# Kernel tuning notes

Measured on AMD Instinct MI355X. Metric: run time of the kernel, lower is better.

The kernel has to match this reference:

```python
import math
import jax, jax.numpy as jnp
import numpy as np

B, S, D = 64, 729, 64  # S = (32*14//16 - 1)**2

def setup_inputs() -> dict:
    key = jax.random.key(0)
    kq, kk, kv, km = jax.random.split(key, 4)
    return {
        "query": jax.random.normal(kq, (B, S, D), dtype=jnp.float32),
        "key": jax.random.normal(kk, (B, S, D), dtype=jnp.float32),
        "value": jax.random.normal(kv, (B, S, D), dtype=jnp.float32),
        "mask": jax.random.randint(km, (B, S, S), 0, 2, dtype=jnp.int32),
    }

def reference(query, key, value, mask):
    dk = query.shape[-1]
    # [B,S,S] scores
    scores = jnp.einsum('bqd,bkd->bqk', query, key) / math.sqrt(dk)
    scores = jnp.where(mask == 0, jnp.float32(-1e9), scores)
    attention = jnp.tanh(scores)  # args.activation == 'tanh'
    # ignore_diag == 1: zero the diagonal of each [S,S] attention map
    eye = jnp.eye(attention.shape[-1], dtype=attention.dtype)
    attention = attention * (1.0 - eye)
    out = jnp.einsum('bqk,bkd->bqd', attention, value)
    return (out, attention)
```

## Files before the change

### kernel.cpp

```cpp
#include <hip/hip_runtime.h>

#define BATCH 64
#define SEQ 729
#define DIM 64
#define NT 12
#define STRB 72
#define STRW 68

typedef __attribute__((ext_vector_type(8))) short bf16x8;
typedef __attribute__((ext_vector_type(4))) float f32x4;
typedef int   i32x4a __attribute__((ext_vector_type(4), aligned(4)));
typedef float f32x4a __attribute__((ext_vector_type(4), aligned(4)));

__device__ __forceinline__ unsigned short f2bf(float f) {
    unsigned int u = __float_as_uint(f);
    u += 0x7fffu + ((u >> 16) & 1u);
    return (unsigned short)(u >> 16);
}

__device__ __forceinline__ unsigned long long pack4bf(float a, float b, float c, float d) {
    return (unsigned long long)f2bf(a)
         | ((unsigned long long)f2bf(b) << 16)
         | ((unsigned long long)f2bf(c) << 32)
         | ((unsigned long long)f2bf(d) << 48);
}

__device__ __forceinline__ float fast_tanh(float x) {
    float e = __builtin_amdgcn_exp2f(x * 2.88539008177792681f);
    return 1.0f - 2.0f * __builtin_amdgcn_rcpf(e + 1.0f);
}

__global__ __launch_bounds__(256, 3) void attn_kernel(
    const float* __restrict__ Qg, const float* __restrict__ Kg,
    const float* __restrict__ Vg, const int* __restrict__ Mg,
    float* __restrict__ Og, float* __restrict__ Ag)
{
    __shared__ unsigned short Ks[64 * STRB];
    __shared__ unsigned short Vs[64 * STRB];
    __shared__ unsigned short Qs[64 * STRB];
    __shared__ float Pf[64 * STRW];
    int* Mint = (int*)Pf;

    const int tid = threadIdx.x;
    const int q0  = blockIdx.x * 64;
    const int b   = blockIdx.y;

    const float* Qb = Qg + (size_t)b * SEQ * DIM;
    const float* Kb = Kg + (size_t)b * SEQ * DIM;
    const float* Vb = Vg + (size_t)b * SEQ * DIM;
    const int*   Mb = Mg + (size_t)b * SEQ * SEQ;
    float* Ob = Og + (size_t)b * SEQ * DIM;
    float* Ab = Ag + (size_t)b * SEQ * SEQ;

    const int lane = tid & 63;
    const int quad = lane >> 4;
    const int l15  = lane & 15;
    const int qrow = (tid >> 6) * 16;

    const int rr = tid >> 4;
    const int cc = (tid & 15) * 4;
    const int vd0 = (tid & 15) * 4;
    const int vk0 = (tid >> 4) * 4;
    const int prow = qrow + (lane >> 4);
    const int pcol = (lane & 15) * 4;

    float4 kr[4], vr[4];
    i32x4a mr[4];

    auto load_k = [&](int k0n) {
        #pragma unroll
        for (int i = 0; i < 4; ++i) {
            int gk = k0n + rr + 16 * i;
            kr[i] = (gk < SEQ) ? *(const float4*)(Kb + gk * DIM + cc)
                               : float4{0, 0, 0, 0};
        }
    };
    auto load_v = [&](int k0n) {
        #pragma unroll
        for (int i = 0; i < 4; ++i) {
            int gk = k0n + vk0 + i;
            vr[i] = (gk < SEQ) ? *(const float4*)(Vb + gk * DIM + vd0)
                               : float4{0, 0, 0, 0};
        }
    };
    auto load_mask = [&](int k0n) {
        #pragma unroll
        for (int i = 0; i < 4; ++i) {
            int gq = q0 + prow + 4 * i;
            int gk = k0n + pcol;
            if (gq < SEQ && gk + 3 < SEQ) {
                mr[i] = *(const i32x4a*)(Mb + (size_t)gq * SEQ + gk);
            } else if (gq < SEQ) {
                i32x4a t;
                #pragma unroll
                for (int e = 0; e < 4; ++e)
                    t[e] = (gk + e < SEQ) ? Mb[(size_t)gq * SEQ + gk + e] : 0;
                mr[i] = t;
            } else {
                mr[i] = i32x4a{0, 0, 0, 0};
            }
        }
    };
    auto drain_mask = [&]() {
        #pragma unroll
        for (int i = 0; i < 4; ++i)
            *(i32x4a*)&Mint[(prow + 4 * i) * STRW + pcol] = mr[i];
    };
    auto drain_kv = [&]() {
        #pragma unroll
        for (int i = 0; i < 4; ++i)
            *(unsigned long long*)&Ks[(rr + 16 * i) * STRB + cc] =
                pack4bf(kr[i].x, kr[i].y, kr[i].z, kr[i].w);
        #pragma unroll
        for (int j = 0; j < 4; ++j) {
            float v0 = j==0?vr[0].x:j==1?vr[0].y:j==2?vr[0].z:vr[0].w;
            float v1 = j==0?vr[1].x:j==1?vr[1].y:j==2?vr[1].z:vr[1].w;
            float v2 = j==0?vr[2].x:j==1?vr[2].y:j==2?vr[2].z:vr[2].w;
            float v3 = j==0?vr[3].x:j==1?vr[3].y:j==2?vr[3].z:vr[3].w;
            *(unsigned long long*)&Vs[(vd0 + j) * STRB + vk0] = pack4bf(v0, v1, v2, v3);
        }
    };

    #pragma unroll
    for (int i = 0; i < 4; ++i) {
        int gq = q0 + rr + 16 * i;
        float4 x = (gq < SEQ) ? *(const float4*)(Qb + gq * DIM + cc)
                              : float4{0, 0, 0, 0};
        *(unsigned long long*)&Qs[(rr + 16 * i) * STRB + cc] = pack4bf(x.x, x.y, x.z, x.w);
    }
    __syncthreads();

    const bf16x8 aq0 = *(const bf16x8*)&Qs[(qrow + l15) * STRB + quad * 8];
    const bf16x8 aq1 = *(const bf16x8*)&Qs[(qrow + l15) * STRB + 32 + quad * 8];

    load_k(0); load_v(0); load_mask(0);

    f32x4 oacc[4];
    #pragma unroll
    for (int dt = 0; dt < 4; ++dt) {
        oacc[dt][0]=0.f; oacc[dt][1]=0.f; oacc[dt][2]=0.f; oacc[dt][3]=0.f;
    }

    for (int kt = 0; kt < NT; ++kt) {
        const int k0 = kt * 64;

        __syncthreads();
        drain_mask();
        drain_kv();
        __syncthreads();

        if (kt + 1 < NT) {
            load_k(k0 + 64); load_v(k0 + 64); load_mask(k0 + 64);
        }

        f32x4 sacc[4];
        #pragma unroll
        for (int nt2 = 0; nt2 < 4; ++nt2) {
            bf16x8 bk0 = *(const bf16x8*)&Ks[(nt2 * 16 + l15) * STRB + quad * 8];
            bf16x8 bk1 = *(const bf16x8*)&Ks[(nt2 * 16 + l15) * STRB + 32 + quad * 8];
            f32x4 c; c[0]=0.f; c[1]=0.f; c[2]=0.f; c[3]=0.f;
            c = __builtin_amdgcn_mfma_f32_16x16x32_bf16(aq0, bk0, c, 0, 0, 0);
            c = __builtin_amdgcn_mfma_f32_16x16x32_bf16(aq1, bk1, c, 0, 0, 0);
            sacc[nt2] = c;
        }

        #pragma unroll
        for (int nt2 = 0; nt2 < 4; ++nt2) {
            int col = nt2 * 16 + l15;
            int gk  = k0 + col;
            #pragma unroll
            for (int r = 0; r < 4; ++r) {
                int qloc = qrow + quad * 4 + r;
                int gq = q0 + qloc;
                int m = Mint[qloc * STRW + col];
                float sv = sacc[nt2][r] * 0.125f;
                bool msk = (m == 0);
                float p = fast_tanh(msk ? -1e9f : sv);
                if (msk) p = -1.0f;
                if (gq == gk) p = 0.0f;
                if (gq >= SEQ || gk >= SEQ) p = 0.0f;
                Pf[qloc * STRW + col] = p;
                Qs[qloc * STRB + col] = f2bf(p);
            }
        }

        #pragma unroll
        for (int i = 0; i < 4; ++i) {
            int row = prow + 4 * i;
            int gq  = q0 + row;
            int gk  = k0 + pcol;
            f32x4 pv = *(const f32x4*)&Pf[row * STRW + pcol];
            if (gq < SEQ) {
                if (gk + 3 < SEQ) {
                    *(f32x4a*)(Ab + (size_t)gq * SEQ + gk) = pv;
                } else {
                    #pragma unroll
                    for (int e = 0; e < 4; ++e)
                        if (gk + e < SEQ) Ab[(size_t)gq * SEQ + gk + e] = pv[e];
                }
            }
        }

        const bf16x8 ap0 = *(const bf16x8*)&Qs[(qrow + l15) * STRB + quad * 8];
        const bf16x8 ap1 = *(const bf16x8*)&Qs[(qrow + l15) * STRB + 32 + quad * 8];
        #pragma unroll
        for (int dt = 0; dt < 4; ++dt) {
            bf16x8 bv0 = *(const bf16x8*)&Vs[(dt * 16 + l15) * STRB + quad * 8];
            bf16x8 bv1 = *(const bf16x8*)&Vs[(dt * 16 + l15) * STRB + 32 + quad * 8];
            oacc[dt] = __builtin_amdgcn_mfma_f32_16x16x32_bf16(ap0, bv0, oacc[dt], 0, 0, 0);
            oacc[dt] = __builtin_amdgcn_mfma_f32_16x16x32_bf16(ap1, bv1, oacc[dt], 0, 0, 0);
        }
    }

    #pragma unroll
    for (int dt = 0; dt < 4; ++dt)
        #pragma unroll
        for (int r = 0; r < 4; ++r)
            Pf[(qrow + quad * 4 + r) * STRW + dt * 16 + l15] = oacc[dt][r];
    #pragma unroll
    for (int i = 0; i < 4; ++i) {
        int row = prow + 4 * i;
        int gq  = q0 + row;
        f32x4 ov = *(const f32x4*)&Pf[row * STRW + pcol];
        if (gq < SEQ) *(f32x4*)(Ob + (size_t)gq * DIM + pcol) = ov;
    }
}

extern "C" void kernel_launch(void* const* d_in, const int* in_sizes, int n_in,
                              void* d_out, int out_size, void* d_ws, size_t ws_size,
                              hipStream_t stream) {
    const float* Q = (const float*)d_in[0];
    const float* K = (const float*)d_in[1];
    const float* V = (const float*)d_in[2];
    const int*   M = (const int*)d_in[3];
    float* Out  = (float*)d_out;
    float* Attn = Out + (size_t)BATCH * SEQ * DIM;
    dim3 grid(NT, BATCH);
    attn_kernel<<<grid, 256, 0, stream>>>(Q, K, V, M, Out, Attn);
}
```

Measured before the change: 328.4 us.

## Split key dimension across blocks with atomic output accumulation and register mask loads

Adds a split-K grid dimension (KSPLIT=2), so each block handles half the key tiles and accumulates its partial output into a zeroed buffer with atomicAdd. Mask values are now loaded straight into MFMA-layout registers with double buffering, and attention values are stored directly from registers. This removes the LDS staging for the mask and the attention output. The aim is more parallelism and less LDS traffic, and launch bounds are raised to 4 blocks per CU. The cost is an extra memset, atomic traffic on the output, and scalar uncoalesced-per-lane mask loads and attention stores.

After: 1.018 ms. +209.8%, slower.

```diff
diff --git a/kernel.cpp b/kernel.cpp
--- a/kernel.cpp
+++ b/kernel.cpp
@@ -3,14 +3,14 @@
 #define BATCH 64
 #define SEQ 729
 #define DIM 64
-#define NT 12
+#define QT 12
+#define NKT 12
+#define KSPLIT 2
+#define KT (NKT / KSPLIT)
 #define STRB 72
-#define STRW 68
 
 typedef __attribute__((ext_vector_type(8))) short bf16x8;
 typedef __attribute__((ext_vector_type(4))) float f32x4;
-typedef int   i32x4a __attribute__((ext_vector_type(4), aligned(4)));
-typedef float f32x4a __attribute__((ext_vector_type(4), aligned(4)));
 
 __device__ __forceinline__ unsigned short f2bf(float f) {
     unsigned int u = __float_as_uint(f);
@@ -30,20 +30,19 @@
     return 1.0f - 2.0f * __builtin_amdgcn_rcpf(e + 1.0f);
 }
 
-__global__ __launch_bounds__(256, 3) void attn_kernel(
+__global__ __launch_bounds__(256, 4) void attn_kernel(
     const float* __restrict__ Qg, const float* __restrict__ Kg,
     const float* __restrict__ Vg, const int* __restrict__ Mg,
     float* __restrict__ Og, float* __restrict__ Ag)
 {
     __shared__ unsigned short Ks[64 * STRB];
     __shared__ unsigned short Vs[64 * STRB];
-    __shared__ unsigned short Qs[64 * STRB];
-    __shared__ float Pf[64 * STRW];
-    int* Mint = (int*)Pf;
+    __shared__ unsigned short Ps[64 * STRB];
 
     const int tid = threadIdx.x;
     const int q0  = blockIdx.x * 64;
     const int b   = blockIdx.y;
+    const int kt0 = blockIdx.z * KT;
 
     const float* Qb = Qg + (size_t)b * SEQ * DIM;
     const float* Kb = Kg + (size_t)b * SEQ * DIM;
@@ -61,11 +60,9 @@
     const int cc = (tid & 15) * 4;
     const int vd0 = (tid & 15) * 4;
     const int vk0 = (tid >> 4) * 4;
-    const int prow = qrow + (lane >> 4);
-    const int pcol = (lane & 15) * 4;
 
     float4 kr[4], vr[4];
-    i32x4a mr[4];
+    int m0[16], m1[16];
 
     auto load_k = [&](int k0n) {
         #pragma unroll
@@ -83,28 +80,19 @@
                                : float4{0, 0, 0, 0};
         }
     };
-    auto load_mask = [&](int k0n) {
-        #pragma unroll
-        for (int i = 0; i < 4; ++i) {
-            int gq = q0 + prow + 4 * i;
-            int gk = k0n + pcol;
-            if (gq < SEQ && gk + 3 < SEQ) {
-                mr[i] = *(const i32x4a*)(Mb + (size_t)gq * SEQ + gk);
-            } else if (gq < SEQ) {
-                i32x4a t;
-                #pragma unroll
-                for (int e = 0; e < 4; ++e)
-                    t[e] = (gk + e < SEQ) ? Mb[(size_t)gq * SEQ + gk + e] : 0;
-                mr[i] = t;
-            } else {
-                mr[i] = i32x4a{0, 0, 0, 0};
+    auto load_mask = [&](int k0n, int (&dst)[16]) {
+        #pragma unroll
+        for (int r = 0; r < 4; ++r) {
+            int gq = q0 + qrow + quad * 4 + r;
+            int cq = gq < SEQ ? gq : SEQ - 1;
+            const int* Mrow = Mb + (size_t)cq * SEQ;
+            #pragma unroll
+            for (int n = 0; n < 4; ++n) {
+                int gk = k0n + n * 16 + l15;
+                int ck = gk < SEQ ? gk : SEQ - 1;
+                dst[r * 4 + n] = Mrow[ck];
             }
         }
-    };
-    auto drain_mask = [&]() {
-        #pragma unroll
-        for (int i = 0; i < 4; ++i)
-            *(i32x4a*)&Mint[(prow + 4 * i) * STRW + pcol] = mr[i];
     };
     auto drain_kv = [&]() {
         #pragma unroll
@@ -126,14 +114,14 @@
         int gq = q0 + rr + 16 * i;
         float4 x = (gq < SEQ) ? *(const float4*)(Qb + gq * DIM + cc)
                               : float4{0, 0, 0, 0};
-        *(unsigned long long*)&Qs[(rr + 16 * i) * STRB + cc] = pack4bf(x.x, x.y, x.z, x.w);
+        *(unsigned long long*)&Ps[(rr + 16 * i) * STRB + cc] = pack4bf(x.x, x.y, x.z, x.w);
     }
     __syncthreads();
 
-    const bf16x8 aq0 = *(const bf16x8*)&Qs[(qrow + l15) * STRB + quad * 8];
-    const bf16x8 aq1 = *(const bf16x8*)&Qs[(qrow + l15) * STRB + 32 + quad * 8];
-
-    load_k(0); load_v(0); load_mask(0);
+    const bf16x8 aq0 = *(const bf16x8*)&Ps[(qrow + l15) * STRB + quad * 8];
+    const bf16x8 aq1 = *(const bf16x8*)&Ps[(qrow + l15) * STRB + 32 + quad * 8];
+
+    load_k(kt0 * 64); load_v(kt0 * 64); load_mask(kt0 * 64, m0);
 
     f32x4 oacc[4];
     #pragma unroll
@@ -141,68 +129,51 @@
         oacc[dt][0]=0.f; oacc[dt][1]=0.f; oacc[dt][2]=0.f; oacc[dt][3]=0.f;
     }
 
-    for (int kt = 0; kt < NT; ++kt) {
-        const int k0 = kt * 64;
+    auto tile = [&](int t, int (&mc)[16], int (&mn)[16]) {
+        const int k0 = (kt0 + t) * 64;
 
         __syncthreads();
-        drain_mask();
         drain_kv();
         __syncthreads();
 
-        if (kt + 1 < NT) {
-            load_k(k0 + 64); load_v(k0 + 64); load_mask(k0 + 64);
+        if (t + 1 < KT) {
+            load_k(k0 + 64); load_v(k0 + 64); load_mask(k0 + 64, mn);
         }
 
         f32x4 sacc[4];
         #pragma unroll
-        for (int nt2 = 0; nt2 < 4; ++nt2) {
-            bf16x8 bk0 = *(const bf16x8*)&Ks[(nt2 * 16 + l15) * STRB + quad * 8];
-            bf16x8 bk1 = *(const bf16x8*)&Ks[(nt2 * 16 + l15) * STRB + 32 + quad * 8];
+        for (int n = 0; n < 4; ++n) {
+            bf16x8 bk0 = *(const bf16x8*)&Ks[(n * 16 + l15) * STRB + quad * 8];
+            bf16x8 bk1 = *(const bf16x8*)&Ks[(n * 16 + l15) * STRB + 32 + quad * 8];
             f32x4 c; c[0]=0.f; c[1]=0.f; c[2]=0.f; c[3]=0.f;
             c = __builtin_amdgcn_mfma_f32_16x16x32_bf16(aq0, bk0, c, 0, 0, 0);
             c = __builtin_amdgcn_mfma_f32_16x16x32_bf16(aq1, bk1, c, 0, 0, 0);
-            sacc[nt2] = c;
-        }
-
-        #pragma unroll
-        for (int nt2 = 0; nt2 < 4; ++nt2) {
-            int col = nt2 * 16 + l15;
-            int gk  = k0 + col;
+            sacc[n] = c;
+        }
+
+        #pragma unroll
+        for (int n = 0; n < 4; ++n) {
+            const int col = n * 16 + l15;
+            const int gk  = k0 + col;
             #pragma unroll
             for (int r = 0; r < 4; ++r) {
-                int qloc = qrow + quad * 4 + r;
-                int gq = q0 + qloc;
-                int m = Mint[qloc * STRW + col];
-                float sv = sacc[nt2][r] * 0.125f;
+                const int qloc = qrow + quad * 4 + r;
+                const int gq   = q0 + qloc;
+                const int m    = mc[r * 4 + n];
+                float sv = sacc[n][r] * 0.125f;
                 bool msk = (m == 0);
                 float p = fast_tanh(msk ? -1e9f : sv);
                 if (msk) p = -1.0f;
                 if (gq == gk) p = 0.0f;
                 if (gq >= SEQ || gk >= SEQ) p = 0.0f;
-                Pf[qloc * STRW + col] = p;
-                Qs[qloc * STRB + col] = f2bf(p);
+                Ps[qloc * STRB + col] = f2bf(p);
+                if (gq < SEQ && gk < SEQ)
+                    Ab[(size_t)gq * SEQ + gk] = p;
             }
         }
 
-        #pragma unroll
-        for (int i = 0; i < 4; ++i) {
-            int row = prow + 4 * i;
-            int gq  = q0 + row;
-            int gk  = k0 + pcol;
-            f32x4 pv = *(const f32x4*)&Pf[row * STRW + pcol];
-            if (gq < SEQ) {
-                if (gk + 3 < SEQ) {
-                    *(f32x4a*)(Ab + (size_t)gq * SEQ + gk) = pv;
-                } else {
-                    #pragma unroll
-                    for (int e = 0; e < 4; ++e)
-                        if (gk + e < SEQ) Ab[(size_t)gq * SEQ + gk + e] = pv[e];
-                }
-            }
-        }
-
-        const bf16x8 ap0 = *(const bf16x8*)&Qs[(qrow + l15) * STRB + quad * 8];
-        const bf16x8 ap1 = *(const bf16x8*)&Qs[(qrow + l15) * STRB + 32 + quad * 8];
+        const bf16x8 ap0 = *(const bf16x8*)&Ps[(qrow + l15) * STRB + quad * 8];
+        const bf16x8 ap1 = *(const bf16x8*)&Ps[(qrow + l15) * STRB + 32 + quad * 8];
         #pragma unroll
         for (int dt = 0; dt < 4; ++dt) {
             bf16x8 bv0 = *(const bf16x8*)&Vs[(dt * 16 + l15) * STRB + quad * 8];
@@ -210,19 +181,21 @@
             oacc[dt] = __builtin_amdgcn_mfma_f32_16x16x32_bf16(ap0, bv0, oacc[dt], 0, 0, 0);
             oacc[dt] = __builtin_amdgcn_mfma_f32_16x16x32_bf16(ap1, bv1, oacc[dt], 0, 0, 0);
         }
+    };
+
+    for (int t = 0; t < KT; t += 2) {
+        tile(t,     m0, m1);
+        tile(t + 1, m1, m0);
     }
 
     #pragma unroll
-    for (int dt = 0; dt < 4; ++dt)
-        #pragma unroll
-        for (int r = 0; r < 4; ++r)
-            Pf[(qrow + quad * 4 + r) * STRW + dt * 16 + l15] = oacc[dt][r];
-    #pragma unroll
-    for (int i = 0; i < 4; ++i) {
-        int row = prow + 4 * i;
-        int gq  = q0 + row;
-        f32x4 ov = *(const f32x4*)&Pf[row * STRW + pcol];
-        if (gq < SEQ) *(f32x4*)(Ob + (size_t)gq * DIM + pcol) = ov;
+    for (int dt = 0; dt < 4; ++dt) {
+        #pragma unroll
+        for (int r = 0; r < 4; ++r) {
+            const int gq = q0 + qrow + quad * 4 + r;
+            if (gq < SEQ)
+                atomicAdd(Ob + (size_t)gq * DIM + dt * 16 + l15, oacc[dt][r]);
+        }
     }
 }
 
@@ -235,6 +208,7 @@
     const int*   M = (const int*)d_in[3];
     float* Out  = (float*)d_out;
     float* Attn = Out + (size_t)BATCH * SEQ * DIM;
-    dim3 grid(NT, BATCH);
+    hipMemsetAsync(Out, 0, (size_t)BATCH * SEQ * DIM * sizeof(float), stream);
+    dim3 grid(QT, BATCH, KSPLIT);
     attn_kernel<<<grid, 256, 0, stream>>>(Q, K, V, M, Out, Attn);
 }
```

## Split key range across blocks with atomic output reduction and slimmer LDS

Applied to the files above, without the earlier changes.

The kernel adds a grid z-dimension that splits the key tiles into two halves per query tile. Each half accumulates partial P·V and adds it into a zeroed output with atomicAdd, after a memset. LDS use is cut by packing the mask into bytes and dropping the fp32 probability staging buffer, and launch bounds are raised to allow more resident blocks. The aim is more parallelism and occupancy to hide memory latency. In exchange, the attention map is now written from bf16-rounded values, which lowers output precision, and atomics plus an extra memset add their own cost.

Measured after the change: 511.1 us. 1.56x slower.

```diff
diff --git a/kernel.cpp b/kernel.cpp
--- a/kernel.cpp
+++ b/kernel.cpp
@@ -3,9 +3,13 @@
 #define BATCH 64
 #define SEQ 729
 #define DIM 64
-#define NT 12
+#define QT 12
+#define NKT 12
+#define KSPLIT 2
+#define KT (NKT / KSPLIT)
 #define STRB 72
-#define STRW 68
+#define MSTR 68
+#define OSTR 68
 
 typedef __attribute__((ext_vector_type(8))) short bf16x8;
 typedef __attribute__((ext_vector_type(4))) float f32x4;
@@ -25,25 +29,31 @@
          | ((unsigned long long)f2bf(d) << 48);
 }
 
+__device__ __forceinline__ float bf2f(unsigned int hi16) {
+    return __uint_as_float(hi16 << 16);
+}
+
 __device__ __forceinline__ float fast_tanh(float x) {
     float e = __builtin_amdgcn_exp2f(x * 2.88539008177792681f);
     return 1.0f - 2.0f * __builtin_amdgcn_rcpf(e + 1.0f);
 }
 
-__global__ __launch_bounds__(256, 3) void attn_kernel(
+__global__ __launch_bounds__(256, 5) void attn_kernel(
     const float* __restrict__ Qg, const float* __restrict__ Kg,
     const float* __restrict__ Vg, const int* __restrict__ Mg,
     float* __restrict__ Og, float* __restrict__ Ag)
 {
-    __shared__ unsigned short Ks[64 * STRB];
-    __shared__ unsigned short Vs[64 * STRB];
-    __shared__ unsigned short Qs[64 * STRB];
-    __shared__ float Pf[64 * STRW];
-    int* Mint = (int*)Pf;
+    __shared__ __align__(16) unsigned char smem[32000];
+    unsigned short* Ks  = (unsigned short*)(smem);
+    unsigned short* Vs  = (unsigned short*)(smem + 9216);
+    unsigned short* Ps  = (unsigned short*)(smem + 18432);
+    unsigned char*  Mb8 = smem + 27648;
+    float* Ostage = (float*)smem;
 
     const int tid = threadIdx.x;
     const int q0  = blockIdx.x * 64;
     const int b   = blockIdx.y;
+    const int kt0 = blockIdx.z * KT;
 
     const float* Qb = Qg + (size_t)b * SEQ * DIM;
     const float* Kb = Kg + (size_t)b * SEQ * DIM;
@@ -103,8 +113,13 @@
     };
     auto drain_mask = [&]() {
         #pragma unroll
-        for (int i = 0; i < 4; ++i)
-            *(i32x4a*)&Mint[(prow + 4 * i) * STRW + pcol] = mr[i];
+        for (int i = 0; i < 4; ++i) {
+            unsigned int mb = (unsigned)(mr[i][0] & 1)
+                            | ((unsigned)(mr[i][1] & 1) << 8)
+                            | ((unsigned)(mr[i][2] & 1) << 16)
+                            | ((unsigned)(mr[i][3] & 1) << 24);
+            *(unsigned int*)&Mb8[(prow + 4 * i) * MSTR + pcol] = mb;
+        }
     };
     auto drain_kv = [&]() {
         #pragma unroll
@@ -126,14 +141,14 @@
         int gq = q0 + rr + 16 * i;
         float4 x = (gq < SEQ) ? *(const float4*)(Qb + gq * DIM + cc)
                               : float4{0, 0, 0, 0};
-        *(unsigned long long*)&Qs[(rr + 16 * i) * STRB + cc] = pack4bf(x.x, x.y, x.z, x.w);
+        *(unsigned long long*)&Ps[(rr + 16 * i) * STRB + cc] = pack4bf(x.x, x.y, x.z, x.w);
     }
     __syncthreads();
 
-    const bf16x8 aq0 = *(const bf16x8*)&Qs[(qrow + l15) * STRB + quad * 8];
-    const bf16x8 aq1 = *(const bf16x8*)&Qs[(qrow + l15) * STRB + 32 + quad * 8];
-
-    load_k(0); load_v(0); load_mask(0);
+    const bf16x8 aq0 = *(const bf16x8*)&Ps[(qrow + l15) * STRB + quad * 8];
+    const bf16x8 aq1 = *(const bf16x8*)&Ps[(qrow + l15) * STRB + 32 + quad * 8];
+
+    load_k(kt0 * 64); load_v(kt0 * 64); load_mask(kt0 * 64);
 
     f32x4 oacc[4];
     #pragma unroll
@@ -141,46 +156,45 @@
         oacc[dt][0]=0.f; oacc[dt][1]=0.f; oacc[dt][2]=0.f; oacc[dt][3]=0.f;
     }
 
-    for (int kt = 0; kt < NT; ++kt) {
-        const int k0 = kt * 64;
+    for (int t = 0; t < KT; ++t) {
+        const int k0 = (kt0 + t) * 64;
 
         __syncthreads();
         drain_mask();
         drain_kv();
         __syncthreads();
 
-        if (kt + 1 < NT) {
+        if (t + 1 < KT) {
             load_k(k0 + 64); load_v(k0 + 64); load_mask(k0 + 64);
         }
 
         f32x4 sacc[4];
         #pragma unroll
-        for (int nt2 = 0; nt2 < 4; ++nt2) {
-            bf16x8 bk0 = *(const bf16x8*)&Ks[(nt2 * 16 + l15) * STRB + quad * 8];
-            bf16x8 bk1 = *(const bf16x8*)&Ks[(nt2 * 16 + l15) * STRB + 32 + quad * 8];
+        for (int n = 0; n < 4; ++n) {
+            bf16x8 bk0 = *(const bf16x8*)&Ks[(n * 16 + l15) * STRB + quad * 8];
+            bf16x8 bk1 = *(const bf16x8*)&Ks[(n * 16 + l15) * STRB + 32 + quad * 8];
             f32x4 c; c[0]=0.f; c[1]=0.f; c[2]=0.f; c[3]=0.f;
             c = __builtin_amdgcn_mfma_f32_16x16x32_bf16(aq0, bk0, c, 0, 0, 0);
             c = __builtin_amdgcn_mfma_f32_16x16x32_bf16(aq1, bk1, c, 0, 0, 0);
-            sacc[nt2] = c;
-        }
-
-        #pragma unroll
-        for (int nt2 = 0; nt2 < 4; ++nt2) {
-            int col = nt2 * 16 + l15;
+            sacc[n] = c;
+        }
+
+        #pragma unroll
+        for (int n = 0; n < 4; ++n) {
+            int col = n * 16 + l15;
             int gk  = k0 + col;
             #pragma unroll
             for (int r = 0; r < 4; ++r) {
                 int qloc = qrow + quad * 4 + r;
                 int gq = q0 + qloc;
-                int m = Mint[qloc * STRW + col];
-                float sv = sacc[nt2][r] * 0.125f;
+                int m = Mb8[qloc * MSTR + col];
+                float sv = sacc[n][r] * 0.125f;
                 bool msk = (m == 0);
                 float p = fast_tanh(msk ? -1e9f : sv);
                 if (msk) p = -1.0f;
                 if (gq == gk) p = 0.0f;
                 if (gq >= SEQ || gk >= SEQ) p = 0.0f;
-                Pf[qloc * STRW + col] = p;
-                Qs[qloc * STRB + col] = f2bf(p);
+                Ps[qloc * STRB + col] = f2bf(p);
             }
         }
 
@@ -189,7 +203,12 @@
             int row = prow + 4 * i;
             int gq  = q0 + row;
             int gk  = k0 + pcol;
-            f32x4 pv = *(const f32x4*)&Pf[row * STRW + pcol];
+            unsigned long long w = *(const unsigned long long*)&Ps[row * STRB + pcol];
+            f32x4 pv;
+            pv[0] = bf2f((unsigned)(w      ) & 0xffffu);
+            pv[1] = bf2f((unsigned)(w >> 16) & 0xffffu);
+            pv[2] = bf2f((unsigned)(w >> 32) & 0xffffu);
+            pv[3] = bf2f((unsigned)(w >> 48) & 0xffffu);
             if (gq < SEQ) {
                 if (gk + 3 < SEQ) {
                     *(f32x4a*)(Ab + (size_t)gq * SEQ + gk) = pv;
@@ -201,8 +220,8 @@
             }
         }
 
-        const bf16x8 ap0 = *(const bf16x8*)&Qs[(qrow + l15) * STRB + quad * 8];
-        const bf16x8 ap1 = *(const bf16x8*)&Qs[(qrow + l15) * STRB + 32 + quad * 8];
+        const bf16x8 ap0 = *(const bf16x8*)&Ps[(qrow + l15) * STRB + quad * 8];
+        const bf16x8 ap1 = *(const bf16x8*)&Ps[(qrow + l15) * STRB + 32 + quad * 8];
         #pragma unroll
         for (int dt = 0; dt < 4; ++dt) {
             bf16x8 bv0 = *(const bf16x8*)&Vs[(dt * 16 + l15) * STRB + quad * 8];
@@ -212,17 +231,19 @@
         }
     }
 
+    __syncthreads();
     #pragma unroll
     for (int dt = 0; dt < 4; ++dt)
         #pragma unroll
         for (int r = 0; r < 4; ++r)
-            Pf[(qrow + quad * 4 + r) * STRW + dt * 16 + l15] = oacc[dt][r];
-    #pragma unroll
-    for (int i = 0; i < 4; ++i) {
-        int row = prow + 4 * i;
+            Ostage[(qrow + quad * 4 + r) * OSTR + dt * 16 + l15] = oacc[dt][r];
+    #pragma unroll
+    for (int r16 = 0; r16 < 16; ++r16) {
+        int row = qrow + r16;
         int gq  = q0 + row;
-        f32x4 ov = *(const f32x4*)&Pf[row * STRW + pcol];
-        if (gq < SEQ) *(f32x4*)(Ob + (size_t)gq * DIM + pcol) = ov;
+        float val = Ostage[row * OSTR + lane];
+        if (gq < SEQ)
+            atomicAdd(Ob + (size_t)gq * DIM + lane, val);
     }
 }
 
@@ -235,6 +256,7 @@
     const int*   M = (const int*)d_in[3];
     float* Out  = (float*)d_out;
     float* Attn = Out + (size_t)BATCH * SEQ * DIM;
-    dim3 grid(NT, BATCH);
+    hipMemsetAsync(Out, 0, (size_t)BATCH * SEQ * DIM * sizeof(float), stream);
+    dim3 grid(QT, BATCH, KSPLIT);
     attn_kernel<<<grid, 256, 0, stream>>>(Q, K, V, M, Out, Attn);
 }
```

## Prefetch K and mask two tiles ahead with double register buffers

Applied to the files above, without the earlier changes.

Moves the K and mask global loads two key tiles ahead using A/B register sets. The loop is unrolled by two so the register names stay static. V is still fetched one tile ahead. This gives more memory latency hiding for the bandwidth-heavy mask stream, at the cost of 32 extra VGPRs, which may lower occupancy under launch_bounds(256,3) or cause spills.

Measured after the change: 425.8 us. 29.6% more time.

```diff
diff --git a/kernel.cpp b/kernel.cpp
--- a/kernel.cpp
+++ b/kernel.cpp
@@ -64,62 +64,123 @@
     const int prow = qrow + (lane >> 4);
     const int pcol = (lane & 15) * 4;
 
-    float4 kr[4], vr[4];
-    i32x4a mr[4];
-
-    auto load_k = [&](int k0n) {
-        #pragma unroll
-        for (int i = 0; i < 4; ++i) {
-            int gk = k0n + rr + 16 * i;
-            kr[i] = (gk < SEQ) ? *(const float4*)(Kb + gk * DIM + cc)
-                               : float4{0, 0, 0, 0};
-        }
-    };
-    auto load_v = [&](int k0n) {
-        #pragma unroll
-        for (int i = 0; i < 4; ++i) {
-            int gk = k0n + vk0 + i;
-            vr[i] = (gk < SEQ) ? *(const float4*)(Vb + gk * DIM + vd0)
-                               : float4{0, 0, 0, 0};
-        }
-    };
-    auto load_mask = [&](int k0n) {
-        #pragma unroll
-        for (int i = 0; i < 4; ++i) {
-            int gq = q0 + prow + 4 * i;
-            int gk = k0n + pcol;
-            if (gq < SEQ && gk + 3 < SEQ) {
-                mr[i] = *(const i32x4a*)(Mb + (size_t)gq * SEQ + gk);
-            } else if (gq < SEQ) {
-                i32x4a t;
-                #pragma unroll
-                for (int e = 0; e < 4; ++e)
-                    t[e] = (gk + e < SEQ) ? Mb[(size_t)gq * SEQ + gk + e] : 0;
-                mr[i] = t;
-            } else {
-                mr[i] = i32x4a{0, 0, 0, 0};
-            }
-        }
-    };
-    auto drain_mask = [&]() {
-        #pragma unroll
-        for (int i = 0; i < 4; ++i)
-            *(i32x4a*)&Mint[(prow + 4 * i) * STRW + pcol] = mr[i];
-    };
-    auto drain_kv = [&]() {
-        #pragma unroll
-        for (int i = 0; i < 4; ++i)
-            *(unsigned long long*)&Ks[(rr + 16 * i) * STRB + cc] =
-                pack4bf(kr[i].x, kr[i].y, kr[i].z, kr[i].w);
-        #pragma unroll
-        for (int j = 0; j < 4; ++j) {
-            float v0 = j==0?vr[0].x:j==1?vr[0].y:j==2?vr[0].z:vr[0].w;
-            float v1 = j==0?vr[1].x:j==1?vr[1].y:j==2?vr[1].z:vr[1].w;
-            float v2 = j==0?vr[2].x:j==1?vr[2].y:j==2?vr[2].z:vr[2].w;
-            float v3 = j==0?vr[3].x:j==1?vr[3].y:j==2?vr[3].z:vr[3].w;
-            *(unsigned long long*)&Vs[(vd0 + j) * STRB + vk0] = pack4bf(v0, v1, v2, v3);
-        }
-    };
+    float4 krA0, krA1, krA2, krA3;
+    float4 krB0, krB1, krB2, krB3;
+    float4 vr0, vr1, vr2, vr3;
+    i32x4a mrA0, mrA1, mrA2, mrA3;
+    i32x4a mrB0, mrB1, mrB2, mrB3;
+
+#define LOAD_K1(k0n, KX, i) { \
+    int gk_ = (k0n) + rr + 16 * (i); \
+    KX = (gk_ < SEQ) ? *(const float4*)(Kb + gk_ * DIM + cc) : float4{0,0,0,0}; }
+#define LOAD_K(k0n, K0,K1,K2,K3) { \
+    LOAD_K1(k0n, K0, 0) LOAD_K1(k0n, K1, 1) LOAD_K1(k0n, K2, 2) LOAD_K1(k0n, K3, 3) }
+
+#define LOAD_V1(k0n, VX, i) { \
+    int gk_ = (k0n) + vk0 + (i); \
+    VX = (gk_ < SEQ) ? *(const float4*)(Vb + gk_ * DIM + vd0) : float4{0,0,0,0}; }
+#define LOAD_V(k0n) { \
+    LOAD_V1(k0n, vr0, 0) LOAD_V1(k0n, vr1, 1) LOAD_V1(k0n, vr2, 2) LOAD_V1(k0n, vr3, 3) }
+
+#define LOAD_M1(k0n, MX, i) { \
+    int gq_ = q0 + prow + 4 * (i); \
+    int gk_ = (k0n) + pcol; \
+    if (gq_ < SEQ && gk_ + 3 < SEQ) { \
+        MX = *(const i32x4a*)(Mb + (size_t)gq_ * SEQ + gk_); \
+    } else if (gq_ < SEQ) { \
+        i32x4a t_; \
+        for (int e_ = 0; e_ < 4; ++e_) \
+            t_[e_] = (gk_ + e_ < SEQ) ? Mb[(size_t)gq_ * SEQ + gk_ + e_] : 0; \
+        MX = t_; \
+    } else { MX = i32x4a{0,0,0,0}; } }
+#define LOAD_M(k0n, M0,M1,M2,M3) { \
+    LOAD_M1(k0n, M0, 0) LOAD_M1(k0n, M1, 1) LOAD_M1(k0n, M2, 2) LOAD_M1(k0n, M3, 3) }
+
+#define DRAIN_M(M0,M1,M2,M3) { \
+    *(i32x4a*)&Mint[(prow +  0) * STRW + pcol] = M0; \
+    *(i32x4a*)&Mint[(prow +  4) * STRW + pcol] = M1; \
+    *(i32x4a*)&Mint[(prow +  8) * STRW + pcol] = M2; \
+    *(i32x4a*)&Mint[(prow + 12) * STRW + pcol] = M3; }
+
+#define DRAIN_K(K0,K1,K2,K3) { \
+    *(unsigned long long*)&Ks[(rr +  0) * STRB + cc] = pack4bf(K0.x, K0.y, K0.z, K0.w); \
+    *(unsigned long long*)&Ks[(rr + 16) * STRB + cc] = pack4bf(K1.x, K1.y, K1.z, K1.w); \
+    *(unsigned long long*)&Ks[(rr + 32) * STRB + cc] = pack4bf(K2.x, K2.y, K2.z, K2.w); \
+    *(unsigned long long*)&Ks[(rr + 48) * STRB + cc] = pack4bf(K3.x, K3.y, K3.z, K3.w); }
+
+#define DRAIN_V() { \
+    *(unsigned long long*)&Vs[(vd0 + 0) * STRB + vk0] = pack4bf(vr0.x, vr1.x, vr2.x, vr3.x); \
+    *(unsigned long long*)&Vs[(vd0 + 1) * STRB + vk0] = pack4bf(vr0.y, vr1.y, vr2.y, vr3.y); \
+    *(unsigned long long*)&Vs[(vd0 + 2) * STRB + vk0] = pack4bf(vr0.z, vr1.z, vr2.z, vr3.z); \
+    *(unsigned long long*)&Vs[(vd0 + 3) * STRB + vk0] = pack4bf(vr0.w, vr1.w, vr2.w, vr3.w); }
+
+#define STEP(kt, K0,K1,K2,K3, M0,M1,M2,M3) { \
+    const int k0_ = (kt) * 64; \
+    __syncthreads();  \
+    DRAIN_M(M0,M1,M2,M3);  \
+    DRAIN_K(K0,K1,K2,K3); \
+    DRAIN_V(); \
+    __syncthreads();  \
+    if ((kt) + 1 < NT) { LOAD_V(k0_ + 64) }                     \
+    if ((kt) + 2 < NT) { LOAD_K(k0_ + 128, K0,K1,K2,K3) \
+                         LOAD_M(k0_ + 128, M0,M1,M2,M3) }       \
+    f32x4 sacc0, sacc1, sacc2, sacc3; \
+    _Pragma("unroll") \
+    for (int n_ = 0; n_ < 4; ++n_) { \
+        bf16x8 bk0 = *(const bf16x8*)&Ks[(n_ * 16 + l15) * STRB + quad * 8]; \
+        bf16x8 bk1 = *(const bf16x8*)&Ks[(n_ * 16 + l15) * STRB + 32 + quad * 8]; \
+        f32x4 c_; c_[0]=0.f; c_[1]=0.f; c_[2]=0.f; c_[3]=0.f; \
+        c_ = __builtin_amdgcn_mfma_f32_16x16x32_bf16(aq0, bk0, c_, 0, 0, 0); \
+        c_ = __builtin_amdgcn_mfma_f32_16x16x32_bf16(aq1, bk1, c_, 0, 0, 0); \
+        if (n_ == 0) sacc0 = c_; else if (n_ == 1) sacc1 = c_; \
+        else if (n_ == 2) sacc2 = c_; else sacc3 = c_; \
+    } \
+    _Pragma("unroll") \
+    for (int n_ = 0; n_ < 4; ++n_) { \
+        f32x4 sv_ = (n_ == 0) ? sacc0 : (n_ == 1) ? sacc1 : (n_ == 2) ? sacc2 : sacc3; \
+        int col_ = n_ * 16 + l15; \
+        int gk_  = k0_ + col_; \
+        _Pragma("unroll") \
+        for (int r_ = 0; r_ < 4; ++r_) { \
+            int qloc_ = qrow + quad * 4 + r_; \
+            int gq_ = q0 + qloc_; \
+            int m_ = Mint[qloc_ * STRW + col_]; \
+            float s_ = sv_[r_] * 0.125f;  \
+            bool msk_ = (m_ == 0); \
+            float p_ = fast_tanh(msk_ ? -1e9f : s_); \
+            if (msk_) p_ = -1.0f; \
+            if (gq_ == gk_) p_ = 0.0f;  \
+            if (gq_ >= SEQ || gk_ >= SEQ) p_ = 0.0f;  \
+            Pf[qloc_ * STRW + col_] = p_;  \
+            Qs[qloc_ * STRB + col_] = f2bf(p_); \
+        } \
+    } \
+    _Pragma("unroll") \
+    for (int i_ = 0; i_ < 4; ++i_) { \
+        int row_ = prow + 4 * i_; \
+        int gq_  = q0 + row_; \
+        int gk_  = k0_ + pcol; \
+        f32x4 pv_ = *(const f32x4*)&Pf[row_ * STRW + pcol]; \
+        if (gq_ < SEQ) { \
+            if (gk_ + 3 < SEQ) { \
+                *(f32x4a*)(Ab + (size_t)gq_ * SEQ + gk_) = pv_; \
+            } else { \
+                for (int e_ = 0; e_ < 4; ++e_) \
+                    if (gk_ + e_ < SEQ) Ab[(size_t)gq_ * SEQ + gk_ + e_] = pv_[e_]; \
+            } \
+        } \
+    } \
+    { \
+        const bf16x8 ap0 = *(const bf16x8*)&Qs[(qrow + l15) * STRB + quad * 8]; \
+        const bf16x8 ap1 = *(const bf16x8*)&Qs[(qrow + l15) * STRB + 32 + quad * 8]; \
+        _Pragma("unroll") \
+        for (int dt_ = 0; dt_ < 4; ++dt_) { \
+            bf16x8 bv0 = *(const bf16x8*)&Vs[(dt_ * 16 + l15) * STRB + quad * 8]; \
+            bf16x8 bv1 = *(const bf16x8*)&Vs[(dt_ * 16 + l15) * STRB + 32 + quad * 8]; \
+            oacc[dt_] = __builtin_amdgcn_mfma_f32_16x16x32_bf16(ap0, bv0, oacc[dt_], 0, 0, 0); \
+            oacc[dt_] = __builtin_amdgcn_mfma_f32_16x16x32_bf16(ap1, bv1, oacc[dt_], 0, 0, 0); \
+        } \
+    } }
 
     #pragma unroll
     for (int i = 0; i < 4; ++i) {
@@ -133,7 +194,11 @@
     const bf16x8 aq0 = *(const bf16x8*)&Qs[(qrow + l15) * STRB + quad * 8];
     const bf16x8 aq1 = *(const bf16x8*)&Qs[(qrow + l15) * STRB + 32 + quad * 8];
 
-    load_k(0); load_v(0); load_mask(0);
+    LOAD_K(0, krA0,krA1,krA2,krA3)
+    LOAD_M(0, mrA0,mrA1,mrA2,mrA3)
+    LOAD_V(0)
+    LOAD_K(64, krB0,krB1,krB2,krB3)
+    LOAD_M(64, mrB0,mrB1,mrB2,mrB3)
 
     f32x4 oacc[4];
     #pragma unroll
@@ -141,75 +206,9 @@
         oacc[dt][0]=0.f; oacc[dt][1]=0.f; oacc[dt][2]=0.f; oacc[dt][3]=0.f;
     }
 
-    for (int kt = 0; kt < NT; ++kt) {
-        const int k0 = kt * 64;
-
-        __syncthreads();
-        drain_mask();
-        drain_kv();
-        __syncthreads();
-
-        if (kt + 1 < NT) {
-            load_k(k0 + 64); load_v(k0 + 64); load_mask(k0 + 64);
-        }
-
-        f32x4 sacc[4];
-        #pragma unroll
-        for (int nt2 = 0; nt2 < 4; ++nt2) {
-            bf16x8 bk0 = *(const bf16x8*)&Ks[(nt2 * 16 + l15) * STRB + quad * 8];
-            bf16x8 bk1 = *(const bf16x8*)&Ks[(nt2 * 16 + l15) * STRB + 32 + quad * 8];
-            f32x4 c; c[0]=0.f; c[1]=0.f; c[2]=0.f; c[3]=0.f;
-            c = __builtin_amdgcn_mfma_f32_16x16x32_bf16(aq0, bk0, c, 0, 0, 0);
-            c = __builtin_amdgcn_mfma_f32_16x16x32_bf16(aq1, bk1, c, 0, 0, 0);
-            sacc[nt2] = c;
-        }
-
-        #pragma unroll
-        for (int nt2 = 0; nt2 < 4; ++nt2) {
-            int col = nt2 * 16 + l15;
-            int gk  = k0 + col;
-            #pragma unroll
-            for (int r = 0; r < 4; ++r) {
-                int qloc = qrow + quad * 4 + r;
-                int gq = q0 + qloc;
-                int m = Mint[qloc * STRW + col];
-                float sv = sacc[nt2][r] * 0.125f;
-                bool msk = (m == 0);
-                float p = fast_tanh(msk ? -1e9f : sv);
-                if (msk) p = -1.0f;
-                if (gq == gk) p = 0.0f;
-                if (gq >= SEQ || gk >= SEQ) p = 0.0f;
-                Pf[qloc * STRW + col] = p;
-                Qs[qloc * STRB + col] = f2bf(p);
-            }
-        }
-
-        #pragma unroll
-        for (int i = 0; i < 4; ++i) {
-            int row = prow + 4 * i;
-            int gq  = q0 + row;
-            int gk  = k0 + pcol;
-            f32x4 pv = *(const f32x4*)&Pf[row * STRW + pcol];
-            if (gq < SEQ) {
-                if (gk + 3 < SEQ) {
-                    *(f32x4a*)(Ab + (size_t)gq * SEQ + gk) = pv;
-                } else {
-                    #pragma unroll
-                    for (int e = 0; e < 4; ++e)
-                        if (gk + e < SEQ) Ab[(size_t)gq * SEQ + gk + e] = pv[e];
-                }
-            }
-        }
-
-        const bf16x8 ap0 = *(const bf16x8*)&Qs[(qrow + l15) * STRB + quad * 8];
-        const bf16x8 ap1 = *(const bf16x8*)&Qs[(qrow + l15) * STRB + 32 + quad * 8];
-        #pragma unroll
-        for (int dt = 0; dt < 4; ++dt) {
-            bf16x8 bv0 = *(const bf16x8*)&Vs[(dt * 16 + l15) * STRB + quad * 8];
-            bf16x8 bv1 = *(const bf16x8*)&Vs[(dt * 16 + l15) * STRB + 32 + quad * 8];
-            oacc[dt] = __builtin_amdgcn_mfma_f32_16x16x32_bf16(ap0, bv0, oacc[dt], 0, 0, 0);
-            oacc[dt] = __builtin_amdgcn_mfma_f32_16x16x32_bf16(ap1, bv1, oacc[dt], 0, 0, 0);
-        }
+    for (int kt = 0; kt < NT; kt += 2) {
+        STEP(kt,     krA0,krA1,krA2,krA3, mrA0,mrA1,mrA2,mrA3)
+        STEP(kt + 1, krB0,krB1,krB2,krB3, mrB0,mrB1,mrB2,mrB3)
     }
 
     #pragma unroll
```
